# Optimization experiments

Hardware: AMD Instinct MI355X
Metric: run time of the kernel (lower is better)

## Reference

```python
import jax, jax.numpy as jnp
import numpy as np

N_WAY = 64
TEMPERATURE = 1.0


def setup_inputs() -> dict:
    key = jax.random.key(0)
    ks = jax.random.split(key, 8)
    T, S, Q, D_IN, H, D_EMB = 16, 2048, 2048, 256, 512, 128
    return {
        "support_x": jax.random.normal(ks[0], (T, S, D_IN), dtype=jnp.float32),
        "support_ids": jax.random.randint(ks[1], (T, S), 0, N_WAY, dtype=jnp.int32),
        "query_x": jax.random.normal(ks[2], (T, Q, D_IN), dtype=jnp.float32),
        "query_y": jax.random.normal(ks[3], (T, Q, D_EMB), dtype=jnp.float32),
        "W1": jax.random.normal(ks[4], (D_IN, H), dtype=jnp.float32) * (1.0 / np.sqrt(D_IN)),
        "b1": jnp.zeros((H,), dtype=jnp.float32),
        "W2": jax.random.normal(ks[5], (H, D_EMB), dtype=jnp.float32) * (1.0 / np.sqrt(H)),
        "b2": jnp.zeros((D_EMB,), dtype=jnp.float32),
    }


def reference(support_x, support_ids, query_x, query_y, W1, b1, W2, b2):
    def embed(x):  # 2-layer MLP embedding network
        return jnp.maximum(x @ W1 + b1, 0.0) @ W2 + b2

    se = embed(support_x)   # [T, S, D]
    qe = embed(query_x)     # [T, Q, D]

    # segment-mean prototypes per class (vectorized scatter-mean)
    onehot = jax.nn.one_hot(support_ids, N_WAY, dtype=se.dtype)      # [T, S, C]
    counts = onehot.sum(axis=1)                                       # [T, C]
    proto_sum = jnp.einsum('tsc,tsd->tcd', onehot, se)                # [T, C, D]
    protos = proto_sum / jnp.maximum(counts, 1.0)[..., None]          # [T, C, D]

    # euclidean cdist via expansion
    q2 = jnp.sum(qe * qe, axis=-1, keepdims=True)                     # [T, Q, 1]
    p2 = jnp.sum(protos * protos, axis=-1)[:, None, :]                # [T, 1, C]
    qp = jnp.einsum('tqd,tcd->tqc', qe, protos)                       # [T, Q, C]
    dist = jnp.sqrt(jnp.maximum(q2 + p2 - 2.0 * qp, 0.0))             # [T, Q, C]

    probs = jax.nn.softmax(-dist / TEMPERATURE, axis=-1)              # [T, Q, C]
    pred = jnp.einsum('tqc,tcd->tqd', probs, protos)                  # [T, Q, D]

    task_losses = jnp.mean((pred - query_y) ** 2, axis=(1, 2))        # [T]
    meta_loss = task_losses.mean()
    return meta_loss
```

## Files before the change

### kernel.cpp

```cpp
#include <hip/hip_runtime.h>
#include <hip/hip_bf16.h>

#define T_TASKS 16
#define S_SUP   2048
#define Q_QRY   2048
#define D_IN    256
#define H_HID   512
#define D_EMB   128
#define N_WAY   64
#define NCHUNK  16
#define CHUNK   128
#define QB      64
#define BM2     64

typedef unsigned short ushortT;
typedef unsigned int uintT;
using bf16x8 = __attribute__((ext_vector_type(8))) short;
using f32x4  = __attribute__((ext_vector_type(4))) float;

__device__ __forceinline__ ushortT f2b(float f) {
    uintT u = __builtin_bit_cast(uintT, f);
    uintT r = u + 0x7FFFu + ((u >> 16) & 1u);
    return (ushortT)(r >> 16);
}
__device__ __forceinline__ float b2f(ushortT h) {
    return __builtin_bit_cast(float, (uintT)h << 16);
}

__global__ __launch_bounds__(256) void convert_weights(
    const float* __restrict__ W1, const float* __restrict__ W2,
    ushortT* __restrict__ W1t, ushortT* __restrict__ W2t)
{
    int i = blockIdx.x * 256 + threadIdx.x;
    if (i < D_IN * H_HID) {
        int k = i >> 9, n = i & 511;
        W1t[n * D_IN + k] = f2b(W1[i]);
    }
    if (i < H_HID * D_EMB) {
        int k = i >> 7, n = i & 127;
        W2t[n * H_HID + k] = f2b(W2[i]);
    }
}

__global__ __launch_bounds__(512, 4) void embed_mfma2(
    const float* __restrict__ xa, const float* __restrict__ xb,
    const ushortT* __restrict__ W1t, const float* __restrict__ b1,
    const ushortT* __restrict__ W2t, const float* __restrict__ b2,
    ushortT* __restrict__ outa, ushortT* __restrict__ outb)
{
    __shared__ ushortT buf[BM2 * H_HID];
    ushortT* xs = buf;
    ushortT* hs = buf;

    const int tid  = threadIdx.x;
    const int wid  = tid >> 6;
    const int lane = tid & 63;
    const int lr   = lane & 15;
    const int lg   = lane >> 4;
    const int bid  = blockIdx.x;
    const float*  x   = (bid < 512) ? xa : xb;
    ushortT*      out = (bid < 512) ? outa : outb;
    const long rowbase = (long)(bid & 511) * BM2;

    #pragma unroll
    for (int i = 0; i < 4; ++i) {
        int ci   = tid + 512 * i;
        int row  = ci >> 5;
        int col8 = (ci & 31) << 3;
        const float4* p = (const float4*)(x + (rowbase + row) * D_IN + col8);
        float4 a = p[0], b = p[1];
        uint4 v;
        v.x = (uintT)f2b(a.x) | ((uintT)f2b(a.y) << 16);
        v.y = (uintT)f2b(a.z) | ((uintT)f2b(a.w) << 16);
        v.z = (uintT)f2b(b.x) | ((uintT)f2b(b.y) << 16);
        v.w = (uintT)f2b(b.z) | ((uintT)f2b(b.w) << 16);
        int idx = (row << 8) + col8;
        idx ^= (row & 7) << 3;
        *(uint4*)&xs[idx] = v;
    }
    __syncthreads();

    f32x4 acc[4][4];
    #pragma unroll
    for (int n = 0; n < 4; ++n) {
        float bv = b1[wid * 64 + n * 16 + lr];
        f32x4 b4 = {bv, bv, bv, bv};
        #pragma unroll
        for (int m = 0; m < 4; ++m) acc[m][n] = b4;
    }
    {
        const ushortT* w1base = W1t + (wid * 64 + lr) * D_IN + lg * 8;
        #pragma unroll
        for (int kk = 0; kk < 8; ++kk) {
            bf16x8 af[4];
            #pragma unroll
            for (int m = 0; m < 4; ++m) {
                int row = m * 16 + lr;
                int idx = (row << 8) + kk * 32 + lg * 8;
                idx ^= (row & 7) << 3;
                af[m] = *(const bf16x8*)&xs[idx];
            }
            #pragma unroll
            for (int n = 0; n < 4; ++n) {
                bf16x8 bf = *(const bf16x8*)(w1base + (n * 16) * D_IN + kk * 32);
                #pragma unroll
                for (int m = 0; m < 4; ++m)
                    acc[m][n] = __builtin_amdgcn_mfma_f32_16x16x32_bf16(af[m], bf, acc[m][n], 0, 0, 0);
            }
        }
    }
    __syncthreads();

    #pragma unroll
    for (int m = 0; m < 4; ++m) {
        #pragma unroll
        for (int n = 0; n < 4; ++n) {
            int col = wid * 64 + n * 16 + lr;
            #pragma unroll
            for (int r = 0; r < 4; ++r) {
                int row = m * 16 + lg * 4 + r;
                float v = fmaxf(acc[m][n][r], 0.0f);
                int idx = row * H_HID + col;
                idx ^= (row & 7) << 3;
                hs[idx] = f2b(v);
            }
        }
    }
    __syncthreads();

    f32x4 acc2[4];
    {
        float bv = b2[wid * 16 + lr];
        f32x4 b4 = {bv, bv, bv, bv};
        #pragma unroll
        for (int m = 0; m < 4; ++m) acc2[m] = b4;
    }
    {
        const ushortT* w2base = W2t + (wid * 16 + lr) * H_HID + lg * 8;
        #pragma unroll
        for (int kk = 0; kk < 16; ++kk) {
            bf16x8 bf = *(const bf16x8*)(w2base + kk * 32);
            #pragma unroll
            for (int m = 0; m < 4; ++m) {
                int row = m * 16 + lr;
                int idx = row * H_HID + kk * 32 + lg * 8;
                idx ^= (row & 7) << 3;
                bf16x8 af = *(const bf16x8*)&hs[idx];
                acc2[m] = __builtin_amdgcn_mfma_f32_16x16x32_bf16(af, bf, acc2[m], 0, 0, 0);
            }
        }
    }
    #pragma unroll
    for (int m = 0; m < 4; ++m)
        #pragma unroll
        for (int r = 0; r < 4; ++r) {
            long row = rowbase + m * 16 + lg * 4 + r;
            out[row * D_EMB + wid * 16 + lr] = f2b(acc2[m][r]);
        }
}

__global__ __launch_bounds__(256) void proto_partial(
    const ushortT* __restrict__ se, const int* __restrict__ ids,
    float* __restrict__ psum, int* __restrict__ pcnt)
{
    __shared__ float acc[2][N_WAY][D_EMB];
    __shared__ int idbuf[CHUNK];

    const int tid  = threadIdx.x;
    const int t    = blockIdx.x >> 4;
    const int ch   = blockIdx.x & 15;
    const int d    = tid & 127;
    const int half = tid >> 7;

    #pragma unroll
    for (int i = 0; i < 64; ++i)
        ((float*)acc)[tid + 256 * i] = 0.0f;
    if (tid < CHUNK) idbuf[tid] = ids[t * S_SUP + ch * CHUNK + tid];
    __syncthreads();

    const ushortT* sb = se + ((long)t * S_SUP + ch * CHUNK) * D_EMB;
    #pragma unroll 4
    for (int s = 0; s < 64; ++s) {
        int row = half * 64 + s;
        int c = idbuf[row];
        acc[half][c][d] += b2f(sb[(long)row * D_EMB + d]);
    }
    __syncthreads();

    float* pb = psum + (long)blockIdx.x * N_WAY * D_EMB;
    #pragma unroll
    for (int i = 0; i < 32; ++i) {
        int idx = tid + 256 * i;
        pb[idx] = acc[0][idx >> 7][idx & 127] + acc[1][idx >> 7][idx & 127];
    }
    if (tid < N_WAY) {
        int cnt = 0;
        #pragma unroll 8
        for (int s = 0; s < CHUNK; ++s) cnt += (idbuf[s] == tid);
        pcnt[blockIdx.x * N_WAY + tid] = cnt;
    }
}

__global__ __launch_bounds__(256) void proto_reduce(
    const float* __restrict__ psum, const int* __restrict__ pcnt,
    float* __restrict__ protos)
{
    int idx = blockIdx.x * 256 + threadIdx.x;
    int t = idx >> 13;
    int cd = idx & 8191;
    int c = cd >> 7;

    float s = 0.0f;
    int cnt = 0;
    #pragma unroll
    for (int ch = 0; ch < NCHUNK; ++ch) {
        s   += psum[((long)(t * NCHUNK + ch)) * N_WAY * D_EMB + cd];
        cnt += pcnt[(t * NCHUNK + ch) * N_WAY + c];
    }
    protos[idx] = s / (float)(cnt > 0 ? cnt : 1);
}

__global__ __launch_bounds__(256) void query_mfma(
    const ushortT* __restrict__ qe, const float* __restrict__ qy,
    const float* __restrict__ protos_g, float* __restrict__ partials)
{
    __shared__ ushortT psA[N_WAY * D_EMB];
    __shared__ ushortT psT[D_EMB * N_WAY];
    __shared__ ushortT probs_s[4][16 * N_WAY];
    __shared__ float p2s[N_WAY];
    __shared__ float wloss[4];

    const int tid  = threadIdx.x;
    const int wave = tid >> 6;
    const int lane = tid & 63;
    const int lr   = lane & 15;
    const int lg   = lane >> 4;
    const int t    = blockIdx.x >> 5;
    const int qblk = blockIdx.x & 31;

    const float* pt = protos_g + (long)t * N_WAY * D_EMB;

    float pp[4];
    #pragma unroll
    for (int i = 0; i < 4; ++i) {
        int ci = tid + 256 * i;
        int c = ci >> 4, col8 = (ci & 15) << 3;
        const float4* p = (const float4*)(pt + c * D_EMB + col8);
        float4 a = p[0], b = p[1];
        ushortT h0 = f2b(a.x), h1 = f2b(a.y), h2 = f2b(a.z), h3 = f2b(a.w);
        ushortT h4 = f2b(b.x), h5 = f2b(b.y), h6 = f2b(b.z), h7 = f2b(b.w);
        float ss = b2f(h0)*b2f(h0) + b2f(h1)*b2f(h1) + b2f(h2)*b2f(h2) + b2f(h3)*b2f(h3)
                 + b2f(h4)*b2f(h4) + b2f(h5)*b2f(h5) + b2f(h6)*b2f(h6) + b2f(h7)*b2f(h7);
        pp[i] = ss;
        uint4 v;
        v.x = (uintT)h0 | ((uintT)h1 << 16);
        v.y = (uintT)h2 | ((uintT)h3 << 16);
        v.z = (uintT)h4 | ((uintT)h5 << 16);
        v.w = (uintT)h6 | ((uintT)h7 << 16);
        int idx = c * D_EMB + col8;
        idx ^= (c & 7) << 3;
        *(uint4*)&psA[idx] = v;
    }
    #pragma unroll
    for (int off = 1; off < 16; off <<= 1) {
        #pragma unroll
        for (int i = 0; i < 4; ++i) pp[i] += __shfl_xor(pp[i], off);
    }
    if ((lane & 15) == 0) {
        int a = wave * 4 + (lane >> 4);
        #pragma unroll
        for (int i = 0; i < 4; ++i) p2s[a + 16 * i] = pp[i];
    }

    {
        int d  = wave * 32 + (lane & 31);
        int ch = lane >> 5;
        #pragma unroll
        for (int m = 0; m < 4; ++m) {
            ushortT h[8];
            #pragma unroll
            for (int j = 0; j < 8; ++j)
                h[j] = f2b(pt[(ch * 32 + m * 8 + j) * D_EMB + d]);
            uint4 v;
            v.x = (uintT)h[0] | ((uintT)h[1] << 16);
            v.y = (uintT)h[2] | ((uintT)h[3] << 16);
            v.z = (uintT)h[4] | ((uintT)h[5] << 16);
            v.w = (uintT)h[6] | ((uintT)h[7] << 16);
            int idx = d * N_WAY + ch * 32 + m * 8;
            idx ^= (d & 7) << 3;
            *(uint4*)&psT[idx] = v;
        }
    }
    __syncthreads();

    const long qrow = (long)t * Q_QRY + qblk * QB + wave * 16 + lr;
    bf16x8 bq[4];
    float q2 = 0.0f;
    #pragma unroll
    for (int kk = 0; kk < 4; ++kk) {
        bq[kk] = *(const bf16x8*)(qe + qrow * D_EMB + kk * 32 + lg * 8);
        #pragma unroll
        for (int j = 0; j < 8; ++j) {
            float v = b2f((ushortT)bq[kk][j]);
            q2 += v * v;
        }
    }
    q2 += __shfl_xor(q2, 16);
    q2 += __shfl_xor(q2, 32);

    f32x4 acc[4];
    #pragma unroll
    for (int mt = 0; mt < 4; ++mt) { f32x4 z = {0,0,0,0}; acc[mt] = z; }
    #pragma unroll
    for (int kk = 0; kk < 4; ++kk) {
        #pragma unroll
        for (int mt = 0; mt < 4; ++mt) {
            int c = mt * 16 + lr;
            int idx = (c * D_EMB + kk * 32 + lg * 8) ^ ((c & 7) << 3);
            bf16x8 af = *(const bf16x8*)&psA[idx];
            acc[mt] = __builtin_amdgcn_mfma_f32_16x16x32_bf16(af, bq[kk], acc[mt], 0, 0, 0);
        }
    }

    float ev[4][4];
    float mx = -1e30f;
    #pragma unroll
    for (int mt = 0; mt < 4; ++mt) {
        #pragma unroll
        for (int r = 0; r < 4; ++r) {
            int c = mt * 16 + lg * 4 + r;
            float d2 = q2 + p2s[c] - 2.0f * acc[mt][r];
            float v = -sqrtf(fmaxf(d2, 0.0f));
            ev[mt][r] = v;
            mx = fmaxf(mx, v);
        }
    }
    mx = fmaxf(mx, __shfl_xor(mx, 16));
    mx = fmaxf(mx, __shfl_xor(mx, 32));
    float sum = 0.0f;
    #pragma unroll
    for (int mt = 0; mt < 4; ++mt)
        #pragma unroll
        for (int r = 0; r < 4; ++r) {
            float e = __expf(ev[mt][r] - mx);
            ev[mt][r] = e;
            sum += e;
        }
    sum += __shfl_xor(sum, 16);
    sum += __shfl_xor(sum, 32);
    float inv = 1.0f / sum;

    #pragma unroll
    for (int mt = 0; mt < 4; ++mt) {
        uintT lo = (uintT)f2b(ev[mt][0] * inv) | ((uintT)f2b(ev[mt][1] * inv) << 16);
        uintT hi = (uintT)f2b(ev[mt][2] * inv) | ((uintT)f2b(ev[mt][3] * inv) << 16);
        int idx = lr * N_WAY + ((mt * 16 + lg * 4) ^ ((lr & 7) << 3));
        uint2 v = {lo, hi};
        *(uint2*)&probs_s[wave][idx] = v;
    }

    f32x4 acc2[8];
    #pragma unroll
    for (int nt = 0; nt < 8; ++nt) { f32x4 z = {0,0,0,0}; acc2[nt] = z; }
    #pragma unroll
    for (int kk = 0; kk < 2; ++kk) {
        int idxa = lr * N_WAY + ((kk * 32 + lg * 8) ^ ((lr & 7) << 3));
        bf16x8 af = *(const bf16x8*)&probs_s[wave][idxa];
        #pragma unroll
        for (int nt = 0; nt < 8; ++nt) {
            int d = nt * 16 + lr;
            int idxb = (d * N_WAY + kk * 32 + lg * 8) ^ ((d & 7) << 3);
            bf16x8 bf = *(const bf16x8*)&psT[idxb];
            acc2[nt] = __builtin_amdgcn_mfma_f32_16x16x32_bf16(af, bf, acc2[nt], 0, 0, 0);
        }
    }

    float lossacc = 0.0f;
    const long qgbase = (long)t * Q_QRY + qblk * QB + wave * 16;
    #pragma unroll
    for (int r = 0; r < 4; ++r) {
        const float* yrow = qy + (qgbase + lg * 4 + r) * D_EMB;
        #pragma unroll
        for (int nt = 0; nt < 8; ++nt) {
            float diff = acc2[nt][r] - yrow[nt * 16 + lr];
            lossacc += diff * diff;
        }
    }
    #pragma unroll
    for (int off = 32; off >= 1; off >>= 1) lossacc += __shfl_xor(lossacc, off);
    if (lane == 0) wloss[wave] = lossacc;
    __syncthreads();
    if (tid == 0)
        partials[blockIdx.x] = wloss[0] + wloss[1] + wloss[2] + wloss[3];
}

__global__ __launch_bounds__(256) void reduce_kernel(
    const float* __restrict__ partials, float* __restrict__ out)
{
    __shared__ float wsum[4];
    const int tid = threadIdx.x;
    float s = partials[tid] + partials[tid + 256];
    #pragma unroll
    for (int off = 32; off >= 1; off >>= 1) s += __shfl_xor(s, off);
    if ((tid & 63) == 0) wsum[tid >> 6] = s;
    __syncthreads();
    if (tid == 0) {
        const float inv = 1.0f / ((float)T_TASKS * Q_QRY * D_EMB);
        out[0] = (wsum[0] + wsum[1] + wsum[2] + wsum[3]) * inv;
    }
}

extern "C" void kernel_launch(void* const* d_in, const int* in_sizes, int n_in,
                              void* d_out, int out_size, void* d_ws, size_t ws_size,
                              hipStream_t stream)
{
    const float* support_x = (const float*)d_in[0];
    const int*   support_ids = (const int*)d_in[1];
    const float* query_x  = (const float*)d_in[2];
    const float* query_y  = (const float*)d_in[3];
    const float* W1 = (const float*)d_in[4];
    const float* b1 = (const float*)d_in[5];
    const float* W2 = (const float*)d_in[6];
    const float* b2 = (const float*)d_in[7];

    ushortT* se     = (ushortT*)d_ws;
    ushortT* qe     = se + (long)T_TASKS * S_SUP * D_EMB;
    float* protos   = (float*)(qe + (long)T_TASKS * Q_QRY * D_EMB);
    float* partials = protos + T_TASKS * N_WAY * D_EMB;
    ushortT* W1t    = (ushortT*)(partials + 1024);
    ushortT* W2t    = W1t + H_HID * D_IN;
    float* psum     = (float*)(W2t + D_EMB * H_HID);
    int*   pcnt     = (int*)(psum + (long)T_TASKS * NCHUNK * N_WAY * D_EMB);

    convert_weights<<<512, 256, 0, stream>>>(W1, W2, W1t, W2t);
    embed_mfma2<<<1024, 512, 0, stream>>>(support_x, query_x, W1t, b1, W2t, b2, se, qe);
    proto_partial<<<T_TASKS * NCHUNK, 256, 0, stream>>>(se, support_ids, psum, pcnt);
    proto_reduce<<<512, 256, 0, stream>>>(psum, pcnt, protos);
    query_mfma<<<T_TASKS * (Q_QRY / QB), 256, 0, stream>>>(qe, query_y, protos, partials);
    reduce_kernel<<<1, 256, 0, stream>>>(partials, (float*)d_out);
}
```

Measured before the change: 86.97 us.

## Shrink embed tile to 32 rows and load inputs directly into MFMA fragments

The MLP embedding kernel now uses 32-row tiles with 256 threads per block across twice as many blocks. The input rows are read from global memory and converted to bf16 straight into MFMA operand registers, skipping the LDS staging and one barrier. Each wave covers more hidden and output columns. This cuts LDS use per block and may raise occupancy, but each W1/W2 fragment is reused over fewer rows, so weight traffic per row roughly doubles, and the uncoalesced strided float loads from x may cost bandwidth.

```diff
diff --git a/kernel.cpp b/kernel.cpp
--- a/kernel.cpp
+++ b/kernel.cpp
@@ -11,7 +11,7 @@
 #define NCHUNK  16
 #define CHUNK   128
 #define QB      64
-#define BM2     64
+#define BM3     32
 
 typedef unsigned short ushortT;
 typedef unsigned int uintT;
@@ -42,15 +42,13 @@
     }
 }
 
-__global__ __launch_bounds__(512, 4) void embed_mfma2(
+__global__ __launch_bounds__(256, 4) void embed_mfma3(
     const float* __restrict__ xa, const float* __restrict__ xb,
     const ushortT* __restrict__ W1t, const float* __restrict__ b1,
     const ushortT* __restrict__ W2t, const float* __restrict__ b2,
     ushortT* __restrict__ outa, ushortT* __restrict__ outb)
 {
-    __shared__ ushortT buf[BM2 * H_HID];
-    ushortT* xs = buf;
-    ushortT* hs = buf;
+    __shared__ ushortT hs[BM3 * H_HID];
 
     const int tid  = threadIdx.x;
     const int wid  = tid >> 6;
@@ -58,104 +56,95 @@
     const int lr   = lane & 15;
     const int lg   = lane >> 4;
     const int bid  = blockIdx.x;
-    const float*  x   = (bid < 512) ? xa : xb;
-    ushortT*      out = (bid < 512) ? outa : outb;
-    const long rowbase = (long)(bid & 511) * BM2;
-
-    #pragma unroll
-    for (int i = 0; i < 4; ++i) {
-        int ci   = tid + 512 * i;
-        int row  = ci >> 5;
-        int col8 = (ci & 31) << 3;
-        const float4* p = (const float4*)(x + (rowbase + row) * D_IN + col8);
-        float4 a = p[0], b = p[1];
-        uint4 v;
-        v.x = (uintT)f2b(a.x) | ((uintT)f2b(a.y) << 16);
-        v.y = (uintT)f2b(a.z) | ((uintT)f2b(a.w) << 16);
-        v.z = (uintT)f2b(b.x) | ((uintT)f2b(b.y) << 16);
-        v.w = (uintT)f2b(b.z) | ((uintT)f2b(b.w) << 16);
-        int idx = (row << 8) + col8;
-        idx ^= (row & 7) << 3;
-        *(uint4*)&xs[idx] = v;
-    }
-    __syncthreads();
-
-    f32x4 acc[4][4];
-    #pragma unroll
-    for (int n = 0; n < 4; ++n) {
-        float bv = b1[wid * 64 + n * 16 + lr];
+    const float*  x   = (bid < 1024) ? xa : xb;
+    ushortT*      out = (bid < 1024) ? outa : outb;
+    const long rowbase = (long)(bid & 1023) * BM3;
+    const float* xbase = x + rowbase * D_IN;
+
+    f32x4 acc[2][8];
+    #pragma unroll
+    for (int n = 0; n < 8; ++n) {
+        float bv = b1[wid * 128 + n * 16 + lr];
         f32x4 b4 = {bv, bv, bv, bv};
-        #pragma unroll
-        for (int m = 0; m < 4; ++m) acc[m][n] = b4;
+        acc[0][n] = b4; acc[1][n] = b4;
     }
     {
-        const ushortT* w1base = W1t + (wid * 64 + lr) * D_IN + lg * 8;
+        const ushortT* w1base = W1t + (wid * 128 + lr) * D_IN + lg * 8;
         #pragma unroll
         for (int kk = 0; kk < 8; ++kk) {
-            bf16x8 af[4];
-            #pragma unroll
-            for (int m = 0; m < 4; ++m) {
-                int row = m * 16 + lr;
-                int idx = (row << 8) + kk * 32 + lg * 8;
-                idx ^= (row & 7) << 3;
-                af[m] = *(const bf16x8*)&xs[idx];
+            bf16x8 af[2];
+            #pragma unroll
+            for (int m = 0; m < 2; ++m) {
+                const float* p = xbase + (m * 16 + lr) * D_IN + kk * 32 + lg * 8;
+                float4 a = *(const float4*)p;
+                float4 b = *(const float4*)(p + 4);
+                uint4 u;
+                u.x = (uintT)f2b(a.x) | ((uintT)f2b(a.y) << 16);
+                u.y = (uintT)f2b(a.z) | ((uintT)f2b(a.w) << 16);
+                u.z = (uintT)f2b(b.x) | ((uintT)f2b(b.y) << 16);
+                u.w = (uintT)f2b(b.z) | ((uintT)f2b(b.w) << 16);
+                af[m] = __builtin_bit_cast(bf16x8, u);
             }
             #pragma unroll
-            for (int n = 0; n < 4; ++n) {
+            for (int n = 0; n < 8; ++n) {
                 bf16x8 bf = *(const bf16x8*)(w1base + (n * 16) * D_IN + kk * 32);
-                #pragma unroll
-                for (int m = 0; m < 4; ++m)
-                    acc[m][n] = __builtin_amdgcn_mfma_f32_16x16x32_bf16(af[m], bf, acc[m][n], 0, 0, 0);
+                acc[0][n] = __builtin_amdgcn_mfma_f32_16x16x32_bf16(af[0], bf, acc[0][n], 0, 0, 0);
+                acc[1][n] = __builtin_amdgcn_mfma_f32_16x16x32_bf16(af[1], bf, acc[1][n], 0, 0, 0);
             }
         }
     }
-    __syncthreads();
-
-    #pragma unroll
-    for (int m = 0; m < 4; ++m) {
-        #pragma unroll
-        for (int n = 0; n < 4; ++n) {
-            int col = wid * 64 + n * 16 + lr;
+
+    #pragma unroll
+    for (int m = 0; m < 2; ++m) {
+        #pragma unroll
+        for (int n = 0; n < 8; ++n) {
+            int col = wid * 128 + n * 16 + lr;
             #pragma unroll
             for (int r = 0; r < 4; ++r) {
                 int row = m * 16 + lg * 4 + r;
                 float v = fmaxf(acc[m][n][r], 0.0f);
-                int idx = row * H_HID + col;
-                idx ^= (row & 7) << 3;
+                int idx = (row * H_HID + col) ^ ((row & 7) << 3);
                 hs[idx] = f2b(v);
             }
         }
     }
     __syncthreads();
 
-    f32x4 acc2[4];
+    f32x4 acc2[2][2];
+    #pragma unroll
+    for (int n = 0; n < 2; ++n) {
+        float bv = b2[wid * 32 + n * 16 + lr];
+        f32x4 b4 = {bv, bv, bv, bv};
+        acc2[0][n] = b4; acc2[1][n] = b4;
+    }
     {
-        float bv = b2[wid * 16 + lr];
-        f32x4 b4 = {bv, bv, bv, bv};
-        #pragma unroll
-        for (int m = 0; m < 4; ++m) acc2[m] = b4;
-    }
-    {
-        const ushortT* w2base = W2t + (wid * 16 + lr) * H_HID + lg * 8;
+        const ushortT* w2base = W2t + (wid * 32 + lr) * H_HID + lg * 8;
         #pragma unroll
         for (int kk = 0; kk < 16; ++kk) {
-            bf16x8 bf = *(const bf16x8*)(w2base + kk * 32);
-            #pragma unroll
-            for (int m = 0; m < 4; ++m) {
+            bf16x8 af[2];
+            #pragma unroll
+            for (int m = 0; m < 2; ++m) {
                 int row = m * 16 + lr;
-                int idx = row * H_HID + kk * 32 + lg * 8;
-                idx ^= (row & 7) << 3;
-                bf16x8 af = *(const bf16x8*)&hs[idx];
-                acc2[m] = __builtin_amdgcn_mfma_f32_16x16x32_bf16(af, bf, acc2[m], 0, 0, 0);
+                int idx = (row * H_HID + kk * 32 + lg * 8) ^ ((row & 7) << 3);
+                af[m] = *(const bf16x8*)&hs[idx];
             }
-        }
-    }
-    #pragma unroll
-    for (int m = 0; m < 4; ++m)
-        #pragma unroll
-        for (int r = 0; r < 4; ++r) {
-            long row = rowbase + m * 16 + lg * 4 + r;
-            out[row * D_EMB + wid * 16 + lr] = f2b(acc2[m][r]);
+            #pragma unroll
+            for (int n = 0; n < 2; ++n) {
+                bf16x8 bf = *(const bf16x8*)(w2base + (n * 16) * H_HID + kk * 32);
+                acc2[0][n] = __builtin_amdgcn_mfma_f32_16x16x32_bf16(af[0], bf, acc2[0][n], 0, 0, 0);
+                acc2[1][n] = __builtin_amdgcn_mfma_f32_16x16x32_bf16(af[1], bf, acc2[1][n], 0, 0, 0);
+            }
+        }
+    }
+    #pragma unroll
+    for (int m = 0; m < 2; ++m)
+        #pragma unroll
+        for (int n = 0; n < 2; ++n) {
+            int col = wid * 32 + n * 16 + lr;
+            long row0 = rowbase + m * 16 + lg * 4;
+            #pragma unroll
+            for (int r = 0; r < 4; ++r)
+                out[(row0 + r) * D_EMB + col] = f2b(acc2[m][n][r]);
         }
 }
 
@@ -433,7 +422,7 @@
     int*   pcnt     = (int*)(psum + (long)T_TASKS * NCHUNK * N_WAY * D_EMB);
 
     convert_weights<<<512, 256, 0, stream>>>(W1, W2, W1t, W2t);
-    embed_mfma2<<<1024, 512, 0, stream>>>(support_x, query_x, W1t, b1, W2t, b2, se, qe);
+    embed_mfma3<<<2048, 256, 0, stream>>>(support_x, query_x, W1t, b1, W2t, b2, se, qe);
     proto_partial<<<T_TASKS * NCHUNK, 256, 0, stream>>>(se, support_ids, psum, pcnt);
     proto_reduce<<<512, 256, 0, stream>>>(psum, pcnt, protos);
     query_mfma<<<T_TASKS * (Q_QRY / QB), 256, 0, stream>>>(qe, query_y, protos, partials);
```

Result: slower. 152.2 us (+75.0%).

## Split fused embedding MLP into two swapped-operand GEMM kernels over row chunks

Applied to the files above, without the earlier changes.

Replaces the single fused two-layer embedding kernel with separate layer-1 and layer-2 kernels. The hidden activations now go through a global scratch buffer, processed in four chunks of 16384 rows so the buffer can reuse the prototype-sum workspace. Operands are swapped so weights feed the MFMA A side and activations the B side, which lets results be stored as packed bf16 pairs. This aims to lift occupancy, since the old kernel needed 64KB of LDS per block, at the cost of extra global traffic for the hidden layer and eight launches instead of one.

```diff
diff --git a/kernel.cpp b/kernel.cpp
--- a/kernel.cpp
+++ b/kernel.cpp
@@ -11,7 +11,7 @@
 #define NCHUNK  16
 #define CHUNK   128
 #define QB      64
-#define BM2     64
+#define PROWS   16384
 
 typedef unsigned short ushortT;
 typedef unsigned int uintT;
@@ -26,6 +26,9 @@
 __device__ __forceinline__ float b2f(ushortT h) {
     return __builtin_bit_cast(float, (uintT)h << 16);
 }
+__device__ __forceinline__ uintT pk2(float a, float b) {
+    return (uintT)f2b(a) | ((uintT)f2b(b) << 16);
+}
 
 __global__ __launch_bounds__(256) void convert_weights(
     const float* __restrict__ W1, const float* __restrict__ W2,
@@ -42,25 +45,20 @@
     }
 }
 
-__global__ __launch_bounds__(512, 4) void embed_mfma2(
-    const float* __restrict__ xa, const float* __restrict__ xb,
-    const ushortT* __restrict__ W1t, const float* __restrict__ b1,
-    const ushortT* __restrict__ W2t, const float* __restrict__ b2,
-    ushortT* __restrict__ outa, ushortT* __restrict__ outb)
-{
-    __shared__ ushortT buf[BM2 * H_HID];
-    ushortT* xs = buf;
-    ushortT* hs = buf;
+__global__ __launch_bounds__(512) void g1_swapped(
+    const float* __restrict__ x, const ushortT* __restrict__ W1t,
+    const float* __restrict__ b1, ushortT* __restrict__ h)
+{
+    __shared__ ushortT xs[64 * D_IN];
 
     const int tid  = threadIdx.x;
     const int wid  = tid >> 6;
     const int lane = tid & 63;
     const int lr   = lane & 15;
-    const int lg   = lane >> 4;
-    const int bid  = blockIdx.x;
-    const float*  x   = (bid < 512) ? xa : xb;
-    ushortT*      out = (bid < 512) ? outa : outb;
-    const long rowbase = (long)(bid & 511) * BM2;
+    const int g    = lane >> 4;
+    const int cg   = wid >> 1;
+    const int rg   = wid & 1;
+    const long rowbase = (long)blockIdx.x * 64;
 
     #pragma unroll
     for (int i = 0; i < 4; ++i) {
@@ -70,92 +68,94 @@
         const float4* p = (const float4*)(x + (rowbase + row) * D_IN + col8);
         float4 a = p[0], b = p[1];
         uint4 v;
-        v.x = (uintT)f2b(a.x) | ((uintT)f2b(a.y) << 16);
-        v.y = (uintT)f2b(a.z) | ((uintT)f2b(a.w) << 16);
-        v.z = (uintT)f2b(b.x) | ((uintT)f2b(b.y) << 16);
-        v.w = (uintT)f2b(b.z) | ((uintT)f2b(b.w) << 16);
+        v.x = pk2(a.x, a.y);
+        v.y = pk2(a.z, a.w);
+        v.z = pk2(b.x, b.y);
+        v.w = pk2(b.z, b.w);
         int idx = (row << 8) + col8;
         idx ^= (row & 7) << 3;
         *(uint4*)&xs[idx] = v;
     }
     __syncthreads();
 
-    f32x4 acc[4][4];
-    #pragma unroll
-    for (int n = 0; n < 4; ++n) {
-        float bv = b1[wid * 64 + n * 16 + lr];
-        f32x4 b4 = {bv, bv, bv, bv};
-        #pragma unroll
-        for (int m = 0; m < 4; ++m) acc[m][n] = b4;
-    }
-    {
-        const ushortT* w1base = W1t + (wid * 64 + lr) * D_IN + lg * 8;
+    bf16x8 bfc[2][8];
+    #pragma unroll
+    for (int i = 0; i < 2; ++i) {
+        int rl = rg * 32 + i * 16 + lr;
         #pragma unroll
         for (int kk = 0; kk < 8; ++kk) {
-            bf16x8 af[4];
-            #pragma unroll
-            for (int m = 0; m < 4; ++m) {
-                int row = m * 16 + lr;
-                int idx = (row << 8) + kk * 32 + lg * 8;
-                idx ^= (row & 7) << 3;
-                af[m] = *(const bf16x8*)&xs[idx];
-            }
-            #pragma unroll
-            for (int n = 0; n < 4; ++n) {
-                bf16x8 bf = *(const bf16x8*)(w1base + (n * 16) * D_IN + kk * 32);
-                #pragma unroll
-                for (int m = 0; m < 4; ++m)
-                    acc[m][n] = __builtin_amdgcn_mfma_f32_16x16x32_bf16(af[m], bf, acc[m][n], 0, 0, 0);
-            }
-        }
-    }
-    __syncthreads();
-
-    #pragma unroll
-    for (int m = 0; m < 4; ++m) {
-        #pragma unroll
-        for (int n = 0; n < 4; ++n) {
-            int col = wid * 64 + n * 16 + lr;
-            #pragma unroll
-            for (int r = 0; r < 4; ++r) {
-                int row = m * 16 + lg * 4 + r;
-                float v = fmaxf(acc[m][n][r], 0.0f);
-                int idx = row * H_HID + col;
-                idx ^= (row & 7) << 3;
-                hs[idx] = f2b(v);
-            }
-        }
-    }
-    __syncthreads();
-
-    f32x4 acc2[4];
-    {
-        float bv = b2[wid * 16 + lr];
-        f32x4 b4 = {bv, bv, bv, bv};
-        #pragma unroll
-        for (int m = 0; m < 4; ++m) acc2[m] = b4;
-    }
-    {
-        const ushortT* w2base = W2t + (wid * 16 + lr) * H_HID + lg * 8;
-        #pragma unroll
-        for (int kk = 0; kk < 16; ++kk) {
-            bf16x8 bf = *(const bf16x8*)(w2base + kk * 32);
-            #pragma unroll
-            for (int m = 0; m < 4; ++m) {
-                int row = m * 16 + lr;
-                int idx = row * H_HID + kk * 32 + lg * 8;
-                idx ^= (row & 7) << 3;
-                bf16x8 af = *(const bf16x8*)&hs[idx];
-                acc2[m] = __builtin_amdgcn_mfma_f32_16x16x32_bf16(af, bf, acc2[m], 0, 0, 0);
-            }
-        }
-    }
-    #pragma unroll
-    for (int m = 0; m < 4; ++m)
-        #pragma unroll
-        for (int r = 0; r < 4; ++r) {
-            long row = rowbase + m * 16 + lg * 4 + r;
-            out[row * D_EMB + wid * 16 + lr] = f2b(acc2[m][r]);
+            int idx = (rl * D_IN + kk * 32 + g * 8) ^ ((rl & 7) << 3);
+            bfc[i][kk] = *(const bf16x8*)&xs[idx];
+        }
+    }
+
+    #pragma unroll
+    for (int ct8 = 0; ct8 < 8; ++ct8) {
+        int c0 = (cg * 8 + ct8) * 16;
+        float4 bv = *(const float4*)&b1[c0 + g * 4];
+        f32x4 acc0 = {bv.x, bv.y, bv.z, bv.w};
+        f32x4 acc1 = acc0;
+        const ushortT* w1p = W1t + (c0 + lr) * D_IN + g * 8;
+        #pragma unroll
+        for (int kk = 0; kk < 8; ++kk) {
+            bf16x8 af = *(const bf16x8*)(w1p + kk * 32);
+            acc0 = __builtin_amdgcn_mfma_f32_16x16x32_bf16(af, bfc[0][kk], acc0, 0, 0, 0);
+            acc1 = __builtin_amdgcn_mfma_f32_16x16x32_bf16(af, bfc[1][kk], acc1, 0, 0, 0);
+        }
+        uint2 u0, u1;
+        u0.x = pk2(fmaxf(acc0[0], 0.f), fmaxf(acc0[1], 0.f));
+        u0.y = pk2(fmaxf(acc0[2], 0.f), fmaxf(acc0[3], 0.f));
+        u1.x = pk2(fmaxf(acc1[0], 0.f), fmaxf(acc1[1], 0.f));
+        u1.y = pk2(fmaxf(acc1[2], 0.f), fmaxf(acc1[3], 0.f));
+        long r0 = rowbase + rg * 32 + lr;
+        *(uint2*)&h[(r0)      * H_HID + c0 + g * 4] = u0;
+        *(uint2*)&h[(r0 + 16) * H_HID + c0 + g * 4] = u1;
+    }
+}
+
+__global__ __launch_bounds__(256) void g2_swapped(
+    const ushortT* __restrict__ h, const ushortT* __restrict__ W2t,
+    const float* __restrict__ b2, ushortT* __restrict__ out)
+{
+    const int tid  = threadIdx.x;
+    const int wid  = tid >> 6;
+    const int lane = tid & 63;
+    const int lr   = lane & 15;
+    const int g    = lane >> 4;
+    const int dtg  = wid >> 1;
+    const int rtg  = wid & 1;
+    const long r0  = (long)blockIdx.x * 64 + rtg * 32;
+
+    f32x4 acc[4][2];
+    #pragma unroll
+    for (int dtl = 0; dtl < 4; ++dtl) {
+        float4 bv = *(const float4*)&b2[dtg * 64 + dtl * 16 + g * 4];
+        f32x4 a = {bv.x, bv.y, bv.z, bv.w};
+        acc[dtl][0] = a; acc[dtl][1] = a;
+    }
+
+    const ushortT* hp0 = h + (r0 + lr)      * H_HID + g * 8;
+    const ushortT* hp1 = h + (r0 + 16 + lr) * H_HID + g * 8;
+    #pragma unroll
+    for (int kk = 0; kk < 16; ++kk) {
+        bf16x8 bf0 = *(const bf16x8*)(hp0 + kk * 32);
+        bf16x8 bf1 = *(const bf16x8*)(hp1 + kk * 32);
+        #pragma unroll
+        for (int dtl = 0; dtl < 4; ++dtl) {
+            bf16x8 af = *(const bf16x8*)(W2t + (dtg * 64 + dtl * 16 + lr) * H_HID + kk * 32 + g * 8);
+            acc[dtl][0] = __builtin_amdgcn_mfma_f32_16x16x32_bf16(af, bf0, acc[dtl][0], 0, 0, 0);
+            acc[dtl][1] = __builtin_amdgcn_mfma_f32_16x16x32_bf16(af, bf1, acc[dtl][1], 0, 0, 0);
+        }
+    }
+
+    #pragma unroll
+    for (int dtl = 0; dtl < 4; ++dtl)
+        #pragma unroll
+        for (int i = 0; i < 2; ++i) {
+            uint2 u;
+            u.x = pk2(acc[dtl][i][0], acc[dtl][i][1]);
+            u.y = pk2(acc[dtl][i][2], acc[dtl][i][3]);
+            *(uint2*)&out[(r0 + i * 16 + lr) * D_EMB + dtg * 64 + dtl * 16 + g * 4] = u;
         }
 }
 
@@ -277,15 +277,15 @@
         int ch = lane >> 5;
         #pragma unroll
         for (int m = 0; m < 4; ++m) {
-            ushortT h[8];
+            ushortT hh[8];
             #pragma unroll
             for (int j = 0; j < 8; ++j)
-                h[j] = f2b(pt[(ch * 32 + m * 8 + j) * D_EMB + d]);
+                hh[j] = f2b(pt[(ch * 32 + m * 8 + j) * D_EMB + d]);
             uint4 v;
-            v.x = (uintT)h[0] | ((uintT)h[1] << 16);
-            v.y = (uintT)h[2] | ((uintT)h[3] << 16);
-            v.z = (uintT)h[4] | ((uintT)h[5] << 16);
-            v.w = (uintT)h[6] | ((uintT)h[7] << 16);
+            v.x = (uintT)hh[0] | ((uintT)hh[1] << 16);
+            v.y = (uintT)hh[2] | ((uintT)hh[3] << 16);
+            v.z = (uintT)hh[4] | ((uintT)hh[5] << 16);
+            v.w = (uintT)hh[6] | ((uintT)hh[7] << 16);
             int idx = d * N_WAY + ch * 32 + m * 8;
             idx ^= (d & 7) << 3;
             *(uint4*)&psT[idx] = v;
@@ -352,8 +352,8 @@
 
     #pragma unroll
     for (int mt = 0; mt < 4; ++mt) {
-        uintT lo = (uintT)f2b(ev[mt][0] * inv) | ((uintT)f2b(ev[mt][1] * inv) << 16);
-        uintT hi = (uintT)f2b(ev[mt][2] * inv) | ((uintT)f2b(ev[mt][3] * inv) << 16);
+        uintT lo = pk2(ev[mt][0] * inv, ev[mt][1] * inv);
+        uintT hi = pk2(ev[mt][2] * inv, ev[mt][3] * inv);
         int idx = lr * N_WAY + ((mt * 16 + lg * 4) ^ ((lr & 7) << 3));
         uint2 v = {lo, hi};
         *(uint2*)&probs_s[wave][idx] = v;
@@ -423,17 +423,25 @@
     const float* W2 = (const float*)d_in[6];
     const float* b2 = (const float*)d_in[7];
 
-    ushortT* se     = (ushortT*)d_ws;
-    ushortT* qe     = se + (long)T_TASKS * S_SUP * D_EMB;
-    float* protos   = (float*)(qe + (long)T_TASKS * Q_QRY * D_EMB);
-    float* partials = protos + T_TASKS * N_WAY * D_EMB;
-    ushortT* W1t    = (ushortT*)(partials + 1024);
-    ushortT* W2t    = W1t + H_HID * D_IN;
-    float* psum     = (float*)(W2t + D_EMB * H_HID);
-    int*   pcnt     = (int*)(psum + (long)T_TASKS * NCHUNK * N_WAY * D_EMB);
+    ushortT* se   = (ushortT*)d_ws;
+    ushortT* qe   = se + (long)32768 * D_EMB;
+    ushortT* W1t  = qe + (long)32768 * D_EMB;
+    ushortT* W2t  = W1t + H_HID * D_IN;
+    float* protos = (float*)(W2t + D_EMB * H_HID);
+    ushortT* h    = (ushortT*)(protos + T_TASKS * N_WAY * D_EMB);
+    float* psum   = (float*)h;
+    int*   pcnt   = (int*)(psum + (long)256 * N_WAY * D_EMB);
+    float* partials = (float*)(pcnt + 256 * N_WAY);
 
     convert_weights<<<512, 256, 0, stream>>>(W1, W2, W1t, W2t);
-    embed_mfma2<<<1024, 512, 0, stream>>>(support_x, query_x, W1t, b1, W2t, b2, se, qe);
+
+    for (int p = 0; p < 4; ++p) {
+        const float* xsrc = ((p < 2) ? support_x : query_x) + (long)(p & 1) * PROWS * D_IN;
+        ushortT* dst      = ((p < 2) ? se : qe) + (long)(p & 1) * PROWS * D_EMB;
+        g1_swapped<<<PROWS / 64, 512, 0, stream>>>(xsrc, W1t, b1, h);
+        g2_swapped<<<PROWS / 64, 256, 0, stream>>>(h, W2t, b2, dst);
+    }
+
     proto_partial<<<T_TASKS * NCHUNK, 256, 0, stream>>>(se, support_ids, psum, pcnt);
     proto_reduce<<<512, 256, 0, stream>>>(psum, pcnt, protos);
     query_mfma<<<T_TASKS * (Q_QRY / QB), 256, 0, stream>>>(qe, query_y, protos, partials);
```

Measured after the change: 188.4 us. 117% more time.
